# Performance work log

Hardware: AMD Instinct MI355X
Metric: run time of the kernel (lower is better)

## Reference

```python
import jax, jax.numpy as jnp
import numpy as np

K = 1024          # n_embeddings
D = 64            # embedding_dim
BETA = 0.25
DECAY = 0.99
EPS = 1e-05
DIVERSITY = 0.8


def setup_inputs() -> dict:
    key = jax.random.key(0)
    k1, k2 = jax.random.split(key)
    x = jax.random.normal(k1, (32, 64, 64, 64), dtype=jnp.float32)
    embeddings = jax.random.normal(k2, (K, D), dtype=jnp.float32)
    return {
        "x": x,
        "embeddings": embeddings,
        "temperature": jnp.ones((), dtype=jnp.float32),
        "ema_cluster_size": jnp.zeros((K,), dtype=jnp.float32),
        "ema_w": jnp.zeros((K, D), dtype=jnp.float32),
        "usage_count": jnp.zeros((K,), dtype=jnp.float32),
    }


def reference(x, embeddings, temperature, ema_cluster_size, ema_w, usage_count):
    sg = jax.lax.stop_gradient
    flat = x.reshape(-1, D)                                   # [N, D]
    # squared euclidean distances: [N, K]
    dist = (jnp.sum(flat * flat, axis=1, keepdims=True)
            + jnp.sum(embeddings * embeddings, axis=1)
            - 2.0 * flat @ embeddings.T)
    enc = jax.nn.softmax(-dist / temperature, axis=1)         # soft assignments [N, K]
    quant = (enc @ embeddings).reshape(x.shape)

    # ---- EMA codebook update (torch does this under no_grad) ----
    enc_sg = sg(enc)
    cluster_counts = jnp.sum(enc_sg, axis=0)                  # [K]
    new_cs = DECAY * ema_cluster_size + (1.0 - DECAY) * cluster_counts
    n = jnp.sum(new_cs)
    cs = (new_cs + EPS) / (n + K * EPS) * n
    dw = enc_sg.T @ sg(flat)                                  # [K, D]
    new_w = DECAY * ema_w + (1.0 - DECAY) * dw
    new_emb = sg(new_w / cs[:, None])                         # updated codebook
    new_usage = sg(0.99 * usage_count + 0.01 * cluster_counts)

    # ---- losses (torch computes losses AFTER the EMA/usage updates) ----
    e_latent = jnp.mean((sg(quant) - x) ** 2)
    q_latent = jnp.mean((quant - sg(x)) ** 2)
    reg = jnp.sum(new_emb ** 2)
    avg_probs = jnp.mean(enc, axis=0)
    entropy = -jnp.sum(avg_probs * jnp.log(avg_probs + 1e-10))
    usage_prob = new_usage / (jnp.sum(new_usage) + 1e-05)
    diversity = -jnp.sum(usage_prob * jnp.log(usage_prob + 1e-10))
    perplexity = jnp.exp(entropy)
    loss = q_latent + BETA * e_latent + reg + DIVERSITY * (entropy + diversity)

    quant_st = x + sg(quant - x)                              # straight-through
    return quant_st, loss, perplexity
```

## Files before the change

### kernel.cpp

```cpp
#include <hip/hip_runtime.h>
#include <stdint.h>

#define NROWS 131072
#define NELEM 8388608

typedef __attribute__((ext_vector_type(8))) short bf16x8;
typedef __attribute__((ext_vector_type(4))) float f32x4;

__device__ __forceinline__ unsigned f2bf(float f) {
  unsigned u = __float_as_uint(f);
  u += 0x7fffu + ((u >> 16) & 1u);
  return u >> 16;
}
__device__ __forceinline__ void split2(float f, unsigned short& hi, unsigned short& lo) {
  unsigned uh = f2bf(f);
  hi = (unsigned short)uh;
  lo = (unsigned short)f2bf(f - __uint_as_float(uh << 16));
}
__device__ __forceinline__ void pack8(const float* v, bf16x8& h8, bf16x8& l8) {
  #pragma unroll
  for (int i = 0; i < 8; ++i) {
    unsigned uh = f2bf(v[i]);
    unsigned ul = f2bf(v[i] - __uint_as_float(uh << 16));
    h8[i] = (short)uh; l8[i] = (short)ul;
  }
}
__device__ __forceinline__ int swz(int row, int bcol) {
  return row * 128 + (bcol ^ ((row & 7) << 4));
}
__device__ __forceinline__ f32x4 mfma3(bf16x8 ah, bf16x8 al, bf16x8 bh, bf16x8 bl, f32x4 c) {
  c = __builtin_amdgcn_mfma_f32_16x16x32_bf16(al, bh, c, 0, 0, 0);
  c = __builtin_amdgcn_mfma_f32_16x16x32_bf16(ah, bl, c, 0, 0, 0);
  c = __builtin_amdgcn_mfma_f32_16x16x32_bf16(ah, bh, c, 0, 0, 0);
  return c;
}
__device__ __forceinline__ void gl16(const void* g, void* l) {
  __builtin_amdgcn_global_load_lds((const __attribute__((address_space(1))) void*)g,
                                   (__attribute__((address_space(3))) void*)l, 16, 0, 0);
}

__global__ void prep_emb(const float* __restrict__ emb, const float* __restrict__ temp,
                         char* __restrict__ erh, char* __restrict__ erl,
                         char* __restrict__ eth, char* __restrict__ etl,
                         float* __restrict__ en2s)
{
  __shared__ __align__(16) float ef[64 * 64];
  const int c = blockIdx.x, t = threadIdx.x;
  const float4* g4 = (const float4*)(emb + (size_t)c * 4096);
  {
    int r = t >> 2, q0 = (t & 3) << 2;
    #pragma unroll
    for (int i = 0; i < 4; ++i) *(float4*)(ef + r * 64 + ((q0 + i) << 2)) = g4[r * 16 + q0 + i];
  }
  __syncthreads();
  char* ph = erh + c * 8192;  char* pl = erl + c * 8192;
  {
    int r = t >> 2, d0 = (t & 3) << 4;
    bf16x8 h8, l8;
    pack8(ef + r * 64 + d0, h8, l8);
    *(bf16x8*)(ph + swz(r, 2 * d0)) = h8;  *(bf16x8*)(pl + swz(r, 2 * d0)) = l8;
    pack8(ef + r * 64 + d0 + 8, h8, l8);
    *(bf16x8*)(ph + swz(r, 2 * d0 + 16)) = h8;  *(bf16x8*)(pl + swz(r, 2 * d0 + 16)) = l8;
  }
  char* qh = eth + c * 8192;  char* ql = etl + c * 8192;
  {
    int d = t >> 2, r0 = (t & 3) << 4;
    float tmp[16];
    #pragma unroll
    for (int i = 0; i < 16; ++i) tmp[i] = ef[(r0 + i) * 64 + d];
    bf16x8 h8, l8;
    pack8(tmp, h8, l8);
    *(bf16x8*)(qh + swz(d, 2 * r0)) = h8;  *(bf16x8*)(ql + swz(d, 2 * r0)) = l8;
    pack8(tmp + 8, h8, l8);
    *(bf16x8*)(qh + swz(d, 2 * r0 + 16)) = h8;  *(bf16x8*)(ql + swz(d, 2 * r0 + 16)) = l8;
  }
  if (t < 64) {
    float s = 0.f;
    #pragma unroll
    for (int j = 0; j < 64; ++j) { float v = ef[t * 64 + j]; s = fmaf(v, v, s); }
    en2s[c * 64 + t] = s / temp[0];
  }
}

__global__ __launch_bounds__(256, 3)
void k_main(const float* __restrict__ x, const float* __restrict__ temp,
            const char* __restrict__ erh, const char* __restrict__ erl,
            const char* __restrict__ eth, const char* __restrict__ etl,
            const float* __restrict__ en2s, float* __restrict__ b_g,
            float* __restrict__ sq_g, float* __restrict__ out)
{
  __shared__ __align__(16) char EB[32768];
  __shared__ __align__(16) char EN[16384];
  __shared__ __align__(16) float en2l[1024];
  __shared__ float fac_l[64];
  __shared__ float linv_l[64];

  const int tid = threadIdx.x;
  const int w = tid >> 6, lane = tid & 63, G = lane >> 4, ln = lane & 15;
  const int row_base = blockIdx.x << 6;
  const float c2 = 2.0f / temp[0];

  {
    const char* gx = (const char*)(x + (size_t)row_base * 64);
    #pragma unroll
    for (int j = 0; j < 4; ++j) gl16(gx + tid * 16 + j * 4096, EN + tid * 16 + j * 4096);
  }
  ((float4*)en2l)[tid] = ((const float4*)en2s)[tid];
  __syncthreads();

  bf16x8 axh[2], axl[2];
  {
    const float* xr = (const float*)EN + (16 * w + ln) * 64;
    float tv[8];
    #pragma unroll
    for (int kt = 0; kt < 2; ++kt) {
      #pragma unroll
      for (int i = 0; i < 8; ++i) tv[i] = xr[32 * kt + 8 * G + i];
      pack8(tv, axh[kt], axl[kt]);
    }
  }

  float m[4], lsum[4];
  #pragma unroll
  for (int r = 0; r < 4; ++r) { m[r] = -3.0e38f; lsum[r] = 0.f; }
  f32x4 qacc[4];
  #pragma unroll
  for (int nt = 0; nt < 4; ++nt) qacc[nt] = (f32x4){0.f, 0.f, 0.f, 0.f};

  for (int c = 0; c < 16; ++c) {
    __syncthreads();
    {
      const char* s0 = erh + c * 8192; const char* s1 = erl + c * 8192;
      const char* s2 = eth + c * 8192; const char* s3 = etl + c * 8192;
      gl16(s0 + tid * 16, EB + tid * 16);
      gl16(s0 + 4096 + tid * 16, EB + 4096 + tid * 16);
      gl16(s1 + tid * 16, EB + 8192 + tid * 16);
      gl16(s1 + 4096 + tid * 16, EB + 12288 + tid * 16);
      gl16(s2 + tid * 16, EB + 16384 + tid * 16);
      gl16(s2 + 4096 + tid * 16, EB + 20480 + tid * 16);
      gl16(s3 + tid * 16, EB + 24576 + tid * 16);
      gl16(s3 + 4096 + tid * 16, EB + 28672 + tid * 16);
    }
    __syncthreads();
    float s[4][4];
    #pragma unroll
    for (int nt = 0; nt < 4; ++nt) {
      f32x4 acc = {0.f, 0.f, 0.f, 0.f};
      #pragma unroll
      for (int kt = 0; kt < 2; ++kt) {
        bf16x8 bh = *(const bf16x8*)(EB + swz(16 * nt + ln, 64 * kt + 16 * G));
        bf16x8 bl = *(const bf16x8*)(EB + 8192 + swz(16 * nt + ln, 64 * kt + 16 * G));
        acc = mfma3(axh[kt], axl[kt], bh, bl, acc);
      }
      float e2 = en2l[(c << 6) + (nt << 4) + ln];
      #pragma unroll
      for (int r = 0; r < 4; ++r) s[nt][r] = fmaf(acc[r], c2, -e2);
    }
    float fac[4];
    #pragma unroll
    for (int r = 0; r < 4; ++r) {
      float cm = fmaxf(fmaxf(s[0][r], s[1][r]), fmaxf(s[2][r], s[3][r]));
      #pragma unroll
      for (int off = 1; off < 16; off <<= 1) cm = fmaxf(cm, __shfl_xor(cm, off, 16));
      float mn = fmaxf(m[r], cm);
      fac[r] = __expf(m[r] - mn);
      float p0 = __expf(s[0][r] - mn), p1 = __expf(s[1][r] - mn);
      float p2 = __expf(s[2][r] - mn), p3 = __expf(s[3][r] - mn);
      s[0][r] = p0; s[1][r] = p1; s[2][r] = p2; s[3][r] = p3;
      float cl = p0 + p1 + p2 + p3;
      #pragma unroll
      for (int off = 1; off < 16; off <<= 1) cl += __shfl_xor(cl, off, 16);
      lsum[r] = lsum[r] * fac[r] + cl;
      m[r] = mn;
    }
    if (ln == 0) {
      #pragma unroll
      for (int r = 0; r < 4; ++r) fac_l[16 * w + 4 * G + r] = fac[r];
    }
    #pragma unroll
    for (int nt = 0; nt < 4; ++nt) {
      #pragma unroll
      for (int r = 0; r < 4; ++r) {
        int row = 16 * w + 4 * G + r, col = 16 * nt + ln;
        unsigned short h, lo2;
        split2(s[nt][r], h, lo2);
        *(unsigned short*)(EN + swz(row, 2 * col)) = h;
        *(unsigned short*)(EN + 8192 + swz(row, 2 * col)) = lo2;
      }
    }
    __syncthreads();
    bf16x8 aeh[2], ael[2];
    #pragma unroll
    for (int kt = 0; kt < 2; ++kt) {
      aeh[kt] = *(const bf16x8*)(EB + 16384 + swz(16 * w + ln, 64 * kt + 16 * G));
      ael[kt] = *(const bf16x8*)(EB + 24576 + swz(16 * w + ln, 64 * kt + 16 * G));
    }
    #pragma unroll
    for (int nt = 0; nt < 4; ++nt) {
      float f = fac_l[16 * nt + ln];
      qacc[nt][0] *= f; qacc[nt][1] *= f; qacc[nt][2] *= f; qacc[nt][3] *= f;
      #pragma unroll
      for (int kt = 0; kt < 2; ++kt) {
        bf16x8 bh = *(const bf16x8*)(EN + swz(16 * nt + ln, 64 * kt + 16 * G));
        bf16x8 bl = *(const bf16x8*)(EN + 8192 + swz(16 * nt + ln, 64 * kt + 16 * G));
        qacc[nt] = mfma3(aeh[kt], ael[kt], bh, bl, qacc[nt]);
      }
    }
  }

  if (ln == 0) {
    #pragma unroll
    for (int r = 0; r < 4; ++r) {
      int row = 16 * w + 4 * G + r;
      linv_l[row] = 1.0f / lsum[r];
      b_g[row_base + row] = m[r] + __logf(lsum[r]);
    }
  }
  __syncthreads();
  float sqp = 0.f;
  #pragma unroll
  for (int nt = 0; nt < 4; ++nt) {
    int row = 16 * nt + ln;
    float li = linv_l[row];
    int d0 = 16 * w + 4 * G;
    float4 x4 = *(const float4*)(x + (size_t)(row_base + row) * 64 + d0);
    float4 q;
    q.x = qacc[nt][0] * li; q.y = qacc[nt][1] * li;
    q.z = qacc[nt][2] * li; q.w = qacc[nt][3] * li;
    *(float4*)(out + (size_t)(row_base + row) * 64 + d0) = q;
    float a = q.x - x4.x, b = q.y - x4.y, cc = q.z - x4.z, d = q.w - x4.w;
    sqp += a * a + b * b + cc * cc + d * d;
  }
  #pragma unroll
  for (int off = 1; off < 64; off <<= 1) sqp += __shfl_xor(sqp, off, 64);
  if (lane == 0) atomicAdd(sq_g, sqp);
}

__global__ __launch_bounds__(256, 3)
void k_dw(const float* __restrict__ x, const float* __restrict__ temp,
          const char* __restrict__ erh, const char* __restrict__ erl,
          const float* __restrict__ en2s, const float* __restrict__ b_g,
          float* __restrict__ dw_g, float* __restrict__ counts_g)
{
  __shared__ __align__(16) float XF[64 * 68];
  __shared__ __align__(16) char XT[16384];
  __shared__ __align__(16) char ET2[16384];
  __shared__ float bs[64];

  const int tid = threadIdx.x;
  const int w = tid >> 6, lane = tid & 63, G = lane >> 4, ln = lane & 15;
  const int kt_blk = blockIdx.x & 15;
  const int rch = blockIdx.x >> 4;
  const int kbase = kt_blk << 6;
  const float c2 = 2.0f / temp[0];

  {
    const char* sh = erh + kt_blk * 8192;
    const char* sl = erl + kt_blk * 8192;
    gl16(sh + tid * 16, ET2 + tid * 16);
    gl16(sh + 4096 + tid * 16, ET2 + 4096 + tid * 16);
    gl16(sl + tid * 16, ET2 + 8192 + tid * 16);
    gl16(sl + 4096 + tid * 16, ET2 + 12288 + tid * 16);
  }
  const float en2v = en2s[kbase + 16 * w + ln];
  __syncthreads();
  bf16x8 beh[2], bel[2];
  #pragma unroll
  for (int kt = 0; kt < 2; ++kt) {
    beh[kt] = *(const bf16x8*)(ET2 + swz(16 * w + ln, 64 * kt + 16 * G));
    bel[kt] = *(const bf16x8*)(ET2 + 8192 + swz(16 * w + ln, 64 * kt + 16 * G));
  }

  f32x4 dwacc[4];
  #pragma unroll
  for (int nt = 0; nt < 4; ++nt) dwacc[nt] = (f32x4){0.f, 0.f, 0.f, 0.f};
  float creg = 0.f;

  const int rows_base = rch << 11;
  for (int t = 0; t < 32; ++t) {
    const int rbase = rows_base + (t << 6);
    __syncthreads();
    {
      const float4* g4 = (const float4*)(x + (size_t)rbase * 64);
      #pragma unroll
      for (int j = 0; j < 4; ++j) {
        int g = tid + (j << 8);
        int row = g >> 4, q = g & 15;
        *(float4*)(XF + row * 68 + (q << 2)) = g4[g];
      }
    }
    if (tid < 64) bs[tid] = b_g[rbase + tid];
    __syncthreads();
    {
      int d = tid & 63, r0 = (tid >> 6) << 4;
      float tmp[16];
      #pragma unroll
      for (int i = 0; i < 16; ++i) tmp[i] = XF[(r0 + i) * 68 + d];
      bf16x8 h8, l8;
      pack8(tmp, h8, l8);
      *(bf16x8*)(XT + swz(d, 2 * r0)) = h8;  *(bf16x8*)(XT + 8192 + swz(d, 2 * r0)) = l8;
      pack8(tmp + 8, h8, l8);
      *(bf16x8*)(XT + swz(d, 2 * r0 + 16)) = h8;  *(bf16x8*)(XT + 8192 + swz(d, 2 * r0 + 16)) = l8;
    }
    float ev[4][4];
    #pragma unroll
    for (int rt = 0; rt < 4; ++rt) {
      const float* xr = XF + (16 * rt + ln) * 68;
      f32x4 acc = {0.f, 0.f, 0.f, 0.f};
      #pragma unroll
      for (int kt = 0; kt < 2; ++kt) {
        float tv[8];
        #pragma unroll
        for (int i = 0; i < 8; ++i) tv[i] = xr[32 * kt + 8 * G + i];
        bf16x8 ah, al;
        pack8(tv, ah, al);
        acc = mfma3(ah, al, beh[kt], bel[kt], acc);
      }
      #pragma unroll
      for (int r = 0; r < 4; ++r) {
        ev[rt][r] = __expf(fmaf(acc[r], c2, -en2v) - bs[16 * rt + 4 * G + r]);
        creg += ev[rt][r];
      }
    }
    #pragma unroll
    for (int rt = 0; rt < 4; ++rt) {
      int code = 16 * w + ln;
      int cb = 2 * (16 * rt + 4 * G);
      unsigned short h0, l0, h1, l1, h2, l2, h3, l3;
      split2(ev[rt][0], h0, l0); split2(ev[rt][1], h1, l1);
      split2(ev[rt][2], h2, l2); split2(ev[rt][3], h3, l3);
      ushort4 hv; hv.x = h0; hv.y = h1; hv.z = h2; hv.w = h3;
      ushort4 lv; lv.x = l0; lv.y = l1; lv.z = l2; lv.w = l3;
      *(ushort4*)(ET2 + swz(code, cb)) = hv;
      *(ushort4*)(ET2 + 8192 + swz(code, cb)) = lv;
    }
    __syncthreads();
    bf16x8 aeh[2], ael[2];
    #pragma unroll
    for (int kt = 0; kt < 2; ++kt) {
      aeh[kt] = *(const bf16x8*)(ET2 + swz(16 * w + ln, 64 * kt + 16 * G));
      ael[kt] = *(const bf16x8*)(ET2 + 8192 + swz(16 * w + ln, 64 * kt + 16 * G));
    }
    #pragma unroll
    for (int nt = 0; nt < 4; ++nt) {
      #pragma unroll
      for (int kt = 0; kt < 2; ++kt) {
        bf16x8 bh = *(const bf16x8*)(XT + swz(16 * nt + ln, 64 * kt + 16 * G));
        bf16x8 bl = *(const bf16x8*)(XT + 8192 + swz(16 * nt + ln, 64 * kt + 16 * G));
        dwacc[nt] = mfma3(aeh[kt], ael[kt], bh, bl, dwacc[nt]);
      }
    }
  }
  #pragma unroll
  for (int nt = 0; nt < 4; ++nt) {
    #pragma unroll
    for (int r = 0; r < 4; ++r) {
      int code = kbase + 16 * w + 4 * G + r;
      int d = 16 * nt + ln;
      atomicAdd(&dw_g[code * 64 + d], dwacc[nt][r]);
    }
  }
  creg += __shfl_xor(creg, 16, 64);
  creg += __shfl_xor(creg, 32, 64);
  if (G == 0) atomicAdd(&counts_g[kbase + 16 * w + ln], creg);
}

__device__ __forceinline__ float blk_sum(float v, float* red4) {
  #pragma unroll
  for (int off = 1; off < 64; off <<= 1) v += __shfl_xor(v, off, 64);
  __syncthreads();
  if ((threadIdx.x & 63) == 0) red4[threadIdx.x >> 6] = v;
  __syncthreads();
  return red4[0] + red4[1] + red4[2] + red4[3];
}

__global__ void k_stats(const float* __restrict__ counts_g, const float* __restrict__ ema_cs,
                        const float* __restrict__ usage, float* __restrict__ cs_g,
                        float* __restrict__ scal)
{
  __shared__ float red4[4];
  const int t = threadIdx.x;
  float4 c4 = ((const float4*)counts_g)[t];
  float4 e4 = ((const float4*)ema_cs)[t];
  float4 u4 = ((const float4*)usage)[t];
  float cnt[4] = {c4.x, c4.y, c4.z, c4.w};
  float ecs[4] = {e4.x, e4.y, e4.z, e4.w};
  float usg[4] = {u4.x, u4.y, u4.z, u4.w};
  float ncs[4], nu[4];
  float n_p = 0.f, snu_p = 0.f, ent_p = 0.f;
  #pragma unroll
  for (int j = 0; j < 4; ++j) {
    ncs[j] = fmaf(0.99f, ecs[j], 0.01f * cnt[j]);
    n_p += ncs[j];
    nu[j] = fmaf(0.99f, usg[j], 0.01f * cnt[j]);
    snu_p += nu[j];
    float avg = cnt[j] * (1.0f / 131072.0f);
    ent_p -= avg * logf(avg + 1e-10f);
  }
  float n = blk_sum(n_p, red4);
  float snu = blk_sum(snu_p, red4);
  float ent = blk_sum(ent_p, red4);
  float div_p = 0.f;
  float denom = n + 1024.0f * 1e-5f;
  float4 cso;
  float* csa = (float*)&cso;
  #pragma unroll
  for (int j = 0; j < 4; ++j) {
    csa[j] = (ncs[j] + 1e-5f) / denom * n;
    float up = nu[j] / (snu + 1e-5f);
    div_p -= up * logf(up + 1e-10f);
  }
  ((float4*)cs_g)[t] = cso;
  float dvr = blk_sum(div_p, red4);
  if (t == 0) { scal[0] = ent; scal[1] = dvr; }
}

__global__ void k_reg(const float* __restrict__ dw_g, const float* __restrict__ ema_w,
                      const float* __restrict__ cs_g, float* __restrict__ reg_g)
{
  int i = (blockIdx.x * 256 + threadIdx.x) * 2;
  float2 d2 = *(const float2*)(dw_g + i);
  float2 w2 = *(const float2*)(ema_w + i);
  float cs = cs_g[i >> 6];
  float v0 = fmaf(0.01f, d2.x, 0.99f * w2.x) / cs;
  float v1 = fmaf(0.01f, d2.y, 0.99f * w2.y) / cs;
  float p = v0 * v0 + v1 * v1;
  #pragma unroll
  for (int off = 1; off < 64; off <<= 1) p += __shfl_xor(p, off, 64);
  if ((threadIdx.x & 63) == 0) atomicAdd(reg_g, p);
}

__global__ void k_out(const float* __restrict__ sq_g, const float* __restrict__ reg_g,
                      const float* __restrict__ scal, float* __restrict__ out)
{
  if (threadIdx.x == 0) {
    float mse = sq_g[0] * (1.0f / 8388608.0f);
    float loss = 1.25f * mse + reg_g[0] + 0.8f * (scal[0] + scal[1]);
    out[NELEM] = loss;
    out[NELEM + 1] = expf(scal[0]);
  }
}

extern "C" void kernel_launch(void* const* d_in, const int* in_sizes, int n_in,
                              void* d_out, int out_size, void* d_ws, size_t ws_size,
                              hipStream_t stream)
{
  const float* x      = (const float*)d_in[0];
  const float* emb    = (const float*)d_in[1];
  const float* temp   = (const float*)d_in[2];
  const float* ema_cs = (const float*)d_in[3];
  const float* ema_w  = (const float*)d_in[4];
  const float* usage  = (const float*)d_in[5];
  float* out = (float*)d_out;
  float* ws  = (float*)d_ws;

  float* counts = ws;
  float* dwv    = ws + 1024;
  float* sq     = ws + 66560;
  float* reg    = ws + 66561;
  float* scal   = ws + 66562;
  float* cs_g   = ws + 66576;
  float* en2s   = ws + 67600;
  float* b_g    = ws + 68624;
  char* erh = (char*)(ws + 199696);
  char* erl = (char*)(ws + 232464);
  char* eth = (char*)(ws + 265232);
  char* etl = (char*)(ws + 298000);

  hipMemsetAsync(ws, 0, 66564 * sizeof(float), stream);
  prep_emb<<<16, 256, 0, stream>>>(emb, temp, erh, erl, eth, etl, en2s);
  k_main<<<NROWS / 64, 256, 0, stream>>>(x, temp, erh, erl, eth, etl, en2s, b_g, sq, out);
  k_dw<<<1024, 256, 0, stream>>>(x, temp, erh, erl, en2s, b_g, dwv, counts);
  k_stats<<<1, 256, 0, stream>>>(counts, ema_cs, usage, cs_g, scal);
  k_reg<<<128, 256, 0, stream>>>(dwv, ema_w, cs_g, reg);
  k_out<<<1, 64, 0, stream>>>(sq, reg, scal, out);
}
```

Measured before the change: 525.0 us.

## Precompute bf16 hi/lo swizzled images of x for the dw kernel

Adds a prep_x kernel that converts x into split bf16 hi/lo images, row-major and transposed, in the swizzled LDS layout, stored in workspace. A new k_dw_fast kernel loads these images straight into LDS with global_load_lds instead of loading fp32 x and converting it in every block, which removes the repeated conversion and transpose work across the 16 code-tile blocks. In exchange it writes and reads 64MB of extra workspace plus an extra kernel launch, and it falls back to the old path when the workspace is too small.

After: 455.3 us. 13.3% less time.

```diff
diff --git a/kernel.cpp b/kernel.cpp
--- a/kernel.cpp
+++ b/kernel.cpp
@@ -39,6 +39,39 @@
                                    (__attribute__((address_space(3))) void*)l, 16, 0, 0);
 }
 
+__device__ __forceinline__ void build_images(const float* __restrict__ src,
+                                             char* __restrict__ rh, char* __restrict__ rl,
+                                             char* __restrict__ th, char* __restrict__ tl,
+                                             float* ef, int t)
+{
+  const float4* g4 = (const float4*)src;
+  {
+    int r = t >> 2, q0 = (t & 3) << 2;
+    #pragma unroll
+    for (int i = 0; i < 4; ++i) *(float4*)(ef + r * 64 + ((q0 + i) << 2)) = g4[r * 16 + q0 + i];
+  }
+  __syncthreads();
+  {
+    int r = t >> 2, d0 = (t & 3) << 4;
+    bf16x8 h8, l8;
+    pack8(ef + r * 64 + d0, h8, l8);
+    *(bf16x8*)(rh + swz(r, 2 * d0)) = h8;  *(bf16x8*)(rl + swz(r, 2 * d0)) = l8;
+    pack8(ef + r * 64 + d0 + 8, h8, l8);
+    *(bf16x8*)(rh + swz(r, 2 * d0 + 16)) = h8;  *(bf16x8*)(rl + swz(r, 2 * d0 + 16)) = l8;
+  }
+  {
+    int d = t >> 2, r0 = (t & 3) << 4;
+    float tmp[16];
+    #pragma unroll
+    for (int i = 0; i < 16; ++i) tmp[i] = ef[(r0 + i) * 64 + d];
+    bf16x8 h8, l8;
+    pack8(tmp, h8, l8);
+    *(bf16x8*)(th + swz(d, 2 * r0)) = h8;  *(bf16x8*)(tl + swz(d, 2 * r0)) = l8;
+    pack8(tmp + 8, h8, l8);
+    *(bf16x8*)(th + swz(d, 2 * r0 + 16)) = h8;  *(bf16x8*)(tl + swz(d, 2 * r0 + 16)) = l8;
+  }
+}
+
 __global__ void prep_emb(const float* __restrict__ emb, const float* __restrict__ temp,
                          char* __restrict__ erh, char* __restrict__ erl,
                          char* __restrict__ eth, char* __restrict__ etl,
@@ -46,40 +79,24 @@
 {
   __shared__ __align__(16) float ef[64 * 64];
   const int c = blockIdx.x, t = threadIdx.x;
-  const float4* g4 = (const float4*)(emb + (size_t)c * 4096);
-  {
-    int r = t >> 2, q0 = (t & 3) << 2;
-    #pragma unroll
-    for (int i = 0; i < 4; ++i) *(float4*)(ef + r * 64 + ((q0 + i) << 2)) = g4[r * 16 + q0 + i];
-  }
-  __syncthreads();
-  char* ph = erh + c * 8192;  char* pl = erl + c * 8192;
-  {
-    int r = t >> 2, d0 = (t & 3) << 4;
-    bf16x8 h8, l8;
-    pack8(ef + r * 64 + d0, h8, l8);
-    *(bf16x8*)(ph + swz(r, 2 * d0)) = h8;  *(bf16x8*)(pl + swz(r, 2 * d0)) = l8;
-    pack8(ef + r * 64 + d0 + 8, h8, l8);
-    *(bf16x8*)(ph + swz(r, 2 * d0 + 16)) = h8;  *(bf16x8*)(pl + swz(r, 2 * d0 + 16)) = l8;
-  }
-  char* qh = eth + c * 8192;  char* ql = etl + c * 8192;
-  {
-    int d = t >> 2, r0 = (t & 3) << 4;
-    float tmp[16];
-    #pragma unroll
-    for (int i = 0; i < 16; ++i) tmp[i] = ef[(r0 + i) * 64 + d];
-    bf16x8 h8, l8;
-    pack8(tmp, h8, l8);
-    *(bf16x8*)(qh + swz(d, 2 * r0)) = h8;  *(bf16x8*)(ql + swz(d, 2 * r0)) = l8;
-    pack8(tmp + 8, h8, l8);
-    *(bf16x8*)(qh + swz(d, 2 * r0 + 16)) = h8;  *(bf16x8*)(ql + swz(d, 2 * r0 + 16)) = l8;
-  }
+  build_images(emb + (size_t)c * 4096, erh + c * 8192, erl + c * 8192,
+               eth + c * 8192, etl + c * 8192, ef, t);
   if (t < 64) {
     float s = 0.f;
     #pragma unroll
     for (int j = 0; j < 64; ++j) { float v = ef[t * 64 + j]; s = fmaf(v, v, s); }
     en2s[c * 64 + t] = s / temp[0];
   }
+}
+
+__global__ void prep_x(const float* __restrict__ x,
+                       char* __restrict__ xrh, char* __restrict__ xrl,
+                       char* __restrict__ xth, char* __restrict__ xtl)
+{
+  __shared__ __align__(16) float ef[64 * 64];
+  const int c = blockIdx.x, t = threadIdx.x;
+  build_images(x + (size_t)c * 4096, xrh + (size_t)c * 8192, xrl + (size_t)c * 8192,
+               xth + (size_t)c * 8192, xtl + (size_t)c * 8192, ef, t);
 }
 
 __global__ __launch_bounds__(256, 3)
@@ -234,6 +251,122 @@
   #pragma unroll
   for (int off = 1; off < 64; off <<= 1) sqp += __shfl_xor(sqp, off, 64);
   if (lane == 0) atomicAdd(sq_g, sqp);
+}
+
+__global__ __launch_bounds__(256, 3)
+void k_dw_fast(const float* __restrict__ temp,
+               const char* __restrict__ erh, const char* __restrict__ erl,
+               const char* __restrict__ xrh, const char* __restrict__ xrl,
+               const char* __restrict__ xth, const char* __restrict__ xtl,
+               const float* __restrict__ en2s, const float* __restrict__ b_g,
+               float* __restrict__ dw_g, float* __restrict__ counts_g)
+{
+  __shared__ __align__(16) char XR[16384];
+  __shared__ __align__(16) char XT[16384];
+  __shared__ __align__(16) char ET2[16384];
+  __shared__ float bs[64];
+
+  const int tid = threadIdx.x;
+  const int w = tid >> 6, lane = tid & 63, G = lane >> 4, ln = lane & 15;
+  const int kt_blk = blockIdx.x & 15;
+  const int rch = blockIdx.x >> 4;
+  const int kbase = kt_blk << 6;
+  const float c2 = 2.0f / temp[0];
+
+  {
+    const char* sh = erh + kt_blk * 8192;
+    const char* sl = erl + kt_blk * 8192;
+    gl16(sh + tid * 16, ET2 + tid * 16);
+    gl16(sh + 4096 + tid * 16, ET2 + 4096 + tid * 16);
+    gl16(sl + tid * 16, ET2 + 8192 + tid * 16);
+    gl16(sl + 4096 + tid * 16, ET2 + 12288 + tid * 16);
+  }
+  const float en2v = en2s[kbase + 16 * w + ln];
+  __syncthreads();
+  bf16x8 beh[2], bel[2];
+  #pragma unroll
+  for (int kt = 0; kt < 2; ++kt) {
+    beh[kt] = *(const bf16x8*)(ET2 + swz(16 * w + ln, 64 * kt + 16 * G));
+    bel[kt] = *(const bf16x8*)(ET2 + 8192 + swz(16 * w + ln, 64 * kt + 16 * G));
+  }
+
+  f32x4 dwacc[4];
+  #pragma unroll
+  for (int nt = 0; nt < 4; ++nt) dwacc[nt] = (f32x4){0.f, 0.f, 0.f, 0.f};
+  float creg = 0.f;
+
+  const int tiles_base = rch << 5;
+  for (int t = 0; t < 32; ++t) {
+    const size_t ib = (size_t)(tiles_base + t) * 8192;
+    const int rbase = (tiles_base + t) << 6;
+    __syncthreads();
+    gl16(xrh + ib + tid * 16, XR + tid * 16);
+    gl16(xrh + ib + 4096 + tid * 16, XR + 4096 + tid * 16);
+    gl16(xrl + ib + tid * 16, XR + 8192 + tid * 16);
+    gl16(xrl + ib + 4096 + tid * 16, XR + 12288 + tid * 16);
+    gl16(xth + ib + tid * 16, XT + tid * 16);
+    gl16(xth + ib + 4096 + tid * 16, XT + 4096 + tid * 16);
+    gl16(xtl + ib + tid * 16, XT + 8192 + tid * 16);
+    gl16(xtl + ib + 4096 + tid * 16, XT + 12288 + tid * 16);
+    if (tid < 64) bs[tid] = b_g[rbase + tid];
+    __syncthreads();
+    float ev[4][4];
+    #pragma unroll
+    for (int rt = 0; rt < 4; ++rt) {
+      f32x4 acc = {0.f, 0.f, 0.f, 0.f};
+      #pragma unroll
+      for (int kt = 0; kt < 2; ++kt) {
+        bf16x8 ah = *(const bf16x8*)(XR + swz(16 * rt + ln, 64 * kt + 16 * G));
+        bf16x8 al = *(const bf16x8*)(XR + 8192 + swz(16 * rt + ln, 64 * kt + 16 * G));
+        acc = mfma3(ah, al, beh[kt], bel[kt], acc);
+      }
+      #pragma unroll
+      for (int r = 0; r < 4; ++r) {
+        ev[rt][r] = __expf(fmaf(acc[r], c2, -en2v) - bs[16 * rt + 4 * G + r]);
+        creg += ev[rt][r];
+      }
+    }
+    #pragma unroll
+    for (int rt = 0; rt < 4; ++rt) {
+      int code = 16 * w + ln;
+      int cb = 2 * (16 * rt + 4 * G);
+      unsigned short h0, l0, h1, l1, h2, l2, h3, l3;
+      split2(ev[rt][0], h0, l0); split2(ev[rt][1], h1, l1);
+      split2(ev[rt][2], h2, l2); split2(ev[rt][3], h3, l3);
+      ushort4 hv; hv.x = h0; hv.y = h1; hv.z = h2; hv.w = h3;
+      ushort4 lv; lv.x = l0; lv.y = l1; lv.z = l2; lv.w = l3;
+      *(ushort4*)(ET2 + swz(code, cb)) = hv;
+      *(ushort4*)(ET2 + 8192 + swz(code, cb)) = lv;
+    }
+    __syncthreads();
+    bf16x8 aeh[2], ael[2];
+    #pragma unroll
+    for (int kt = 0; kt < 2; ++kt) {
+      aeh[kt] = *(const bf16x8*)(ET2 + swz(16 * w + ln, 64 * kt + 16 * G));
+      ael[kt] = *(const bf16x8*)(ET2 + 8192 + swz(16 * w + ln, 64 * kt + 16 * G));
+    }
+    #pragma unroll
+    for (int nt = 0; nt < 4; ++nt) {
+      #pragma unroll
+      for (int kt = 0; kt < 2; ++kt) {
+        bf16x8 bh = *(const bf16x8*)(XT + swz(16 * nt + ln, 64 * kt + 16 * G));
+        bf16x8 bl = *(const bf16x8*)(XT + 8192 + swz(16 * nt + ln, 64 * kt + 16 * G));
+        dwacc[nt] = mfma3(aeh[kt], ael[kt], bh, bl, dwacc[nt]);
+      }
+    }
+  }
+  #pragma unroll
+  for (int nt = 0; nt < 4; ++nt) {
+    #pragma unroll
+    for (int r = 0; r < 4; ++r) {
+      int code = kbase + 16 * w + 4 * G + r;
+      int d = 16 * nt + ln;
+      atomicAdd(&dw_g[code * 64 + d], dwacc[nt][r]);
+    }
+  }
+  creg += __shfl_xor(creg, 16, 64);
+  creg += __shfl_xor(creg, 32, 64);
+  if (G == 0) atomicAdd(&counts_g[kbase + 16 * w + ln], creg);
 }
 
 __global__ __launch_bounds__(256, 3)
@@ -466,11 +599,22 @@
   char* erl = (char*)(ws + 232464);
   char* eth = (char*)(ws + 265232);
   char* etl = (char*)(ws + 298000);
+  char* xrh = (char*)(ws + 330768);
+  char* xrl = xrh + (size_t)16777216;
+  char* xth = xrl + (size_t)16777216;
+  char* xtl = xth + (size_t)16777216;
+  const size_t need_fast = (size_t)330768 * 4 + 4ull * 16777216;
 
   hipMemsetAsync(ws, 0, 66564 * sizeof(float), stream);
   prep_emb<<<16, 256, 0, stream>>>(emb, temp, erh, erl, eth, etl, en2s);
-  k_main<<<NROWS / 64, 256, 0, stream>>>(x, temp, erh, erl, eth, etl, en2s, b_g, sq, out);
-  k_dw<<<1024, 256, 0, stream>>>(x, temp, erh, erl, en2s, b_g, dwv, counts);
+  if (ws_size >= need_fast) {
+    prep_x<<<2048, 256, 0, stream>>>(x, xrh, xrl, xth, xtl);
+    k_main<<<NROWS / 64, 256, 0, stream>>>(x, temp, erh, erl, eth, etl, en2s, b_g, sq, out);
+    k_dw_fast<<<1024, 256, 0, stream>>>(temp, erh, erl, xrh, xrl, xth, xtl, en2s, b_g, dwv, counts);
+  } else {
+    k_main<<<NROWS / 64, 256, 0, stream>>>(x, temp, erh, erl, eth, etl, en2s, b_g, sq, out);
+    k_dw<<<1024, 256, 0, stream>>>(x, temp, erh, erl, en2s, b_g, dwv, counts);
+  }
   k_stats<<<1, 256, 0, stream>>>(counts, ema_cs, usage, cs_g, scal);
   k_reg<<<128, 256, 0, stream>>>(dwv, ema_w, cs_g, reg);
   k_out<<<1, 64, 0, stream>>>(sq, reg, scal, out);
```
